# Kernel optimization log

Hardware: AMD Instinct MI355X
Metric: run time of the kernel (lower is better)

The kernel has to match this reference:

```python
import jax, jax.numpy as jnp
import numpy as np

N = 50000
E = 800000
H = 128
K = 4
BN_EPS = 1e-5


def _cheb_norm(edge_index):
    # PyG ChebConv with normalization='sym', lambda_max=2.0:
    # L_hat = 2L/lambda_max - I = -D^{-1/2} A D^{-1/2}
    src, dst = edge_index[0], edge_index[1]
    deg = jax.ops.segment_sum(jnp.ones((E,), jnp.float32), src, num_segments=N)
    dinv = jnp.where(deg > 0, jax.lax.rsqrt(jnp.maximum(deg, 1.0)), 0.0)
    return -dinv[src] * dinv[dst]  # [E]


def _cheb_conv(x, src, dst, w, W, b):
    # Chebyshev recursion: Tx0=x, Tx1=L_hat x, Txk = 2 L_hat Tx_{k-1} - Tx_{k-2}
    def prop(h):
        return jax.ops.segment_sum(h[src] * w[:, None], dst, num_segments=N)
    Tx0 = x
    out = Tx0 @ W[0]
    Tx1 = prop(Tx0)
    out = out + Tx1 @ W[1]
    for k in range(2, W.shape[0]):
        Tx2 = 2.0 * prop(Tx1) - Tx0
        out = out + Tx2 @ W[k]
        Tx0, Tx1 = Tx1, Tx2
    return out + b


def _bn(h, gamma, beta):
    # BatchNorm1d, training mode: biased batch stats over nodes
    m = h.mean(axis=0)
    v = h.var(axis=0)
    return (h - m) * jax.lax.rsqrt(v + BN_EPS) * gamma + beta


def setup_inputs() -> dict:
    key = jax.random.key(0)
    ks = jax.random.split(key, 8)
    x = jax.random.normal(ks[0], (N, 3), jnp.float32)
    edge_index = jax.random.randint(ks[1], (2, E), 0, N, jnp.int64)
    s1 = 1.0 / np.sqrt(3)
    s2 = 1.0 / np.sqrt(H)
    d = {
        'x': x,
        'edge_index': edge_index,
        'W1': jax.random.normal(ks[2], (K, 3, H), jnp.float32) * s1,
        'b1': jnp.zeros((H,), jnp.float32),
        'W2': jax.random.normal(ks[3], (K, H, H), jnp.float32) * s2,
        'b2': jnp.zeros((H,), jnp.float32),
        'W3': jax.random.normal(ks[4], (K, H, H), jnp.float32) * s2,
        'b3': jnp.zeros((H,), jnp.float32),
        'W4': jax.random.normal(ks[5], (K, H, H), jnp.float32) * s2,
        'b4': jnp.zeros((H,), jnp.float32),
        'g1': jnp.ones((H,), jnp.float32), 'be1': jnp.zeros((H,), jnp.float32),
        'g2': jnp.ones((H,), jnp.float32), 'be2': jnp.zeros((H,), jnp.float32),
        'g3': jnp.ones((H,), jnp.float32), 'be3': jnp.zeros((H,), jnp.float32),
    }
    return d


def reference(x, edge_index, W1, b1, W2, b2, W3, b3, W4, b4, g1, be1, g2, be2, g3, be3):
    src, dst = edge_index[0], edge_index[1]
    w = _cheb_norm(edge_index)
    h = _bn(jax.nn.leaky_relu(_cheb_conv(x, src, dst, w, W1, b1)), g1, be1)
    h = _bn(jax.nn.leaky_relu(_cheb_conv(h, src, dst, w, W2, b2)), g2, be2)
    h = _bn(jax.nn.relu(_cheb_conv(h, src, dst, w, W3, b3)), g3, be3)
    h = _cheb_conv(h, src, dst, w, W4, b4)
    # F.normalize(p=2, dim=1)
    nrm = jnp.sqrt(jnp.sum(h * h, axis=1, keepdims=True))
    return h / jnp.maximum(nrm, 1e-12)
```

## Files before the change

kernel.cpp:

```cpp
#include <hip/hip_runtime.h>
#include <hip/hip_fp16.h>

#define NN 50000
#define NE 800000
#define HD 128
#define NSL 128
#define SLE (NE / NSL)
#define PW  12500

typedef __attribute__((ext_vector_type(8))) short short8;
typedef __attribute__((ext_vector_type(4))) float f32x4;
typedef __attribute__((ext_vector_type(4))) unsigned u32x4;

__device__ inline unsigned bf2pack(float lo, float hi) {
    unsigned a = __float_as_uint(lo); a = (a + 0x7fffu + ((a >> 16) & 1u)) >> 16;
    unsigned b = __float_as_uint(hi); b = (b + 0x7fffu + ((b >> 16) & 1u)) >> 16;
    return a | (b << 16);
}

__device__ inline float edgw(unsigned p) {
    return __half2float(__ushort_as_half((unsigned short)(p >> 16)));
}

__global__ __launch_bounds__(256) void k_hist(const int* __restrict__ ei,
                                              unsigned* __restrict__ phist) {
    __shared__ unsigned hist[PW];
    int b = blockIdx.x;
    int a = b >> 8;
    int s = (b & 255) >> 1;
    int c = b & 1;
    int tid = threadIdx.x;
    for (int i = tid; i < PW; i += 256) hist[i] = 0u;
    __syncthreads();
    const int* arr = ei + a * NE + s * SLE;
    int lo = c * 25000;
    for (int i = tid; i < SLE; i += 256) {
        int v = arr[i] - lo;
        if ((unsigned)v < 25000u)
            atomicAdd(&hist[v >> 1], 1u << ((v & 1) * 16));
    }
    __syncthreads();
    unsigned* dst = phist + (size_t)b * PW;
    for (int i = tid; i < PW; i += 256) dst[i] = hist[i];
}

__global__ __launch_bounds__(256) void k_hreduce(const unsigned* __restrict__ phist,
                                                 float* __restrict__ dinv,
                                                 int* __restrict__ cnt,
                                                 unsigned* __restrict__ pre,
                                                 int* __restrict__ dhist) {
    if (blockIdx.x == 0 && threadIdx.x < 64) dhist[threadIdx.x] = 0;
    int idx = blockIdx.x * 256 + threadIdx.x;
    if (idx >= 50000) return;
    int a = idx / 25000;
    int gw = idx % 25000;
    int c = gw / PW;
    int w = gw % PW;
    unsigned accLo = 0, accHi = 0;
    for (int s = 0; s < NSL; s++) {
        unsigned p = phist[(size_t)(((a * NSL + s) * 2 + c)) * PW + w];
        if (a == 1) pre[(size_t)s * 25000 + gw] = accLo | (accHi << 16);
        accLo += p & 0xffffu;
        accHi += p >> 16;
    }
    int b0 = c * 25000 + 2 * w;
    if (a == 0) {
        dinv[b0]     = accLo ? rsqrtf((float)accLo) : 0.0f;
        dinv[b0 + 1] = accHi ? rsqrtf((float)accHi) : 0.0f;
    } else {
        cnt[b0]     = (int)accLo;
        cnt[b0 + 1] = (int)accHi;
    }
}

__global__ __launch_bounds__(1024) void k_scan1(const int* __restrict__ cnt,
                                                int* __restrict__ rowptr,
                                                int* __restrict__ bsum,
                                                int* __restrict__ dhist) {
    __shared__ int s[1024];
    __shared__ int dh[64];
    int tid = threadIdx.x;
    int gid = blockIdx.x * 1024 + tid;
    int v = (gid < NN) ? cnt[gid] : 0;
    s[tid] = v;
    if (tid < 64) dh[tid] = 0;
    __syncthreads();
    if (gid < NN) atomicAdd(&dh[v < 63 ? v : 63], 1);
    for (int off = 1; off < 1024; off <<= 1) {
        int t = 0;
        if (tid >= off) t = s[tid - off];
        __syncthreads();
        s[tid] += t;
        __syncthreads();
    }
    if (gid < NN) rowptr[gid] = s[tid] - v;
    if (tid == 1023) bsum[blockIdx.x] = s[1023];
    if (tid < 64 && dh[tid]) atomicAdd(&dhist[tid], dh[tid]);
}

__global__ void k_scan2(const int* __restrict__ bsum, int* __restrict__ boff,
                        int nb, int* __restrict__ rowptr,
                        const int* __restrict__ dhist, int* __restrict__ gbase) {
    int lane = threadIdx.x;
    int v = (lane < nb) ? bsum[lane] : 0;
    int s = v;
    #pragma unroll
    for (int off = 1; off < 64; off <<= 1) {
        int t = __shfl_up(s, off, 64);
        if (lane >= off) s += t;
    }
    if (lane < nb) boff[lane] = s - v;
    if (lane == 63) rowptr[NN] = s;
    int d = dhist[lane];
    int sd = d;
    #pragma unroll
    for (int off = 1; off < 64; off <<= 1) {
        int t = __shfl_up(sd, off, 64);
        if (lane >= off) sd += t;
    }
    gbase[lane] = sd - d;
}

__global__ void k_scan3(int* __restrict__ rowptr, const int* __restrict__ boff) {
    int i = blockIdx.x * 256 + threadIdx.x;
    if (i < NN) rowptr[i] += boff[i >> 10];
}

__global__ __launch_bounds__(256) void k_permbuild(const int* __restrict__ cnt,
                                                   int* __restrict__ gbase,
                                                   int* __restrict__ perm) {
    __shared__ int lcnt[64];
    __shared__ int lbase[64];
    int tid = threadIdx.x;
    if (tid < 64) lcnt[tid] = 0;
    __syncthreads();
    int n = blockIdx.x * 256 + tid;
    int r = 0, dg = 0;
    if (n < NN) {
        int v = cnt[n];
        dg = v < 63 ? v : 63;
        r = atomicAdd(&lcnt[dg], 1);
    }
    __syncthreads();
    if (tid < 64 && lcnt[tid]) lbase[tid] = atomicAdd(&gbase[tid], lcnt[tid]);
    __syncthreads();
    if (n < NN) perm[lbase[dg] + r] = n;
}

__global__ __launch_bounds__(256) void k_fill2(const int* __restrict__ ei,
                                               const float* __restrict__ dinv,
                                               const int* __restrict__ rowptr,
                                               const unsigned* __restrict__ pre,
                                               unsigned* __restrict__ edg) {
    __shared__ unsigned rank[PW];
    int b = blockIdx.x;
    int s = b >> 1;
    int c = b & 1;
    int tid = threadIdx.x;
    for (int i = tid; i < PW; i += 256) rank[i] = 0u;
    __syncthreads();
    int lo = c * 25000;
    const unsigned* preS = pre + (size_t)s * 25000 + c * PW;
    for (int i = tid; i < SLE; i += 256) {
        int e = s * SLE + i;
        int d = ei[NE + e];
        int v = d - lo;
        if ((unsigned)v < 25000u) {
            int src = ei[e];
            int w = v >> 1;
            int sh = (v & 1) * 16;
            unsigned r = atomicAdd(&rank[w], 1u << sh);
            r = (r >> sh) & 0xffffu;
            unsigned pw = (preS[w] >> sh) & 0xffffu;
            int pos = rowptr[d] + (int)pw + (int)r;
            unsigned short hw = __half_as_ushort(__float2half(-dinv[src] * dinv[d]));
            edg[pos] = (unsigned)src | ((unsigned)hw << 16);
        }
    }
}

__global__ __launch_bounds__(128) void k_prop3(const float* __restrict__ h,
                        const float* __restrict__ sub,
                        const int* __restrict__ rowptr, const unsigned* __restrict__ edg,
                        const int* __restrict__ perm,
                        float* __restrict__ out) {
    int idx = blockIdx.x * 128 + threadIdx.x;
    if (idx >= NN) return;
    int node = perm[idx];
    int e0 = rowptr[node], e1 = rowptr[node + 1];
    float a0 = 0.f, a1 = 0.f, a2 = 0.f;
    float c0 = 0.f, c1 = 0.f, c2 = 0.f;
    int e = e0;
    for (; e + 4 <= e1; e += 4) {
        unsigned p0 = edg[e], p1 = edg[e + 1], p2 = edg[e + 2], p3 = edg[e + 3];
        int s0 = (int)(p0 & 0xffffu) * 3, s1 = (int)(p1 & 0xffffu) * 3;
        int s2 = (int)(p2 & 0xffffu) * 3, s3 = (int)(p3 & 0xffffu) * 3;
        float x0 = h[s0], y0 = h[s0 + 1], z0 = h[s0 + 2];
        float x1 = h[s1], y1 = h[s1 + 1], z1 = h[s1 + 2];
        float x2 = h[s2], y2 = h[s2 + 1], z2 = h[s2 + 2];
        float x3 = h[s3], y3 = h[s3 + 1], z3 = h[s3 + 2];
        float w0 = edgw(p0), w1 = edgw(p1), w2 = edgw(p2), w3 = edgw(p3);
        a0 = fmaf(w0, x0, a0); a1 = fmaf(w0, y0, a1); a2 = fmaf(w0, z0, a2);
        c0 = fmaf(w1, x1, c0); c1 = fmaf(w1, y1, c1); c2 = fmaf(w1, z1, c2);
        a0 = fmaf(w2, x2, a0); a1 = fmaf(w2, y2, a1); a2 = fmaf(w2, z2, a2);
        c0 = fmaf(w3, x3, c0); c1 = fmaf(w3, y3, c1); c2 = fmaf(w3, z3, c2);
    }
    if (e < e1) {
        unsigned p0 = edg[e];
        unsigned p1 = (e + 1 < e1) ? edg[e + 1] : 0u;
        unsigned p2 = (e + 2 < e1) ? edg[e + 2] : 0u;
        int s0 = (int)(p0 & 0xffffu) * 3, s1 = (int)(p1 & 0xffffu) * 3;
        int s2 = (int)(p2 & 0xffffu) * 3;
        float x0 = h[s0], y0 = h[s0 + 1], z0 = h[s0 + 2];
        float x1 = h[s1], y1 = h[s1 + 1], z1 = h[s1 + 2];
        float x2 = h[s2], y2 = h[s2 + 1], z2 = h[s2 + 2];
        float w0 = edgw(p0), w1 = edgw(p1), w2 = edgw(p2);
        a0 = fmaf(w0, x0, a0); a1 = fmaf(w0, y0, a1); a2 = fmaf(w0, z0, a2);
        c0 = fmaf(w1, x1, c0); c1 = fmaf(w1, y1, c1); c2 = fmaf(w1, z1, c2);
        a0 = fmaf(w2, x2, a0); a1 = fmaf(w2, y2, a1); a2 = fmaf(w2, z2, a2);
    }
    a0 += c0; a1 += c1; a2 += c2;
    if (sub) {
        a0 = 2.f * a0 - sub[node * 3 + 0];
        a1 = 2.f * a1 - sub[node * 3 + 1];
        a2 = 2.f * a2 - sub[node * 3 + 2];
    }
    out[node * 3 + 0] = a0;
    out[node * 3 + 1] = a1;
    out[node * 3 + 2] = a2;
}

#define ACC8(acc, u, v)                                               \
    acc[0] = fmaf(v, __uint_as_float(u[0] << 16), acc[0]);            \
    acc[1] = fmaf(v, __uint_as_float(u[0] & 0xffff0000u), acc[1]);    \
    acc[2] = fmaf(v, __uint_as_float(u[1] << 16), acc[2]);            \
    acc[3] = fmaf(v, __uint_as_float(u[1] & 0xffff0000u), acc[3]);    \
    acc[4] = fmaf(v, __uint_as_float(u[2] << 16), acc[4]);            \
    acc[5] = fmaf(v, __uint_as_float(u[2] & 0xffff0000u), acc[5]);    \
    acc[6] = fmaf(v, __uint_as_float(u[3] << 16), acc[6]);            \
    acc[7] = fmaf(v, __uint_as_float(u[3] & 0xffff0000u), acc[7]);

__global__ __launch_bounds__(256) void k_prop_pl(
        const unsigned short* __restrict__ h, const unsigned short* __restrict__ sub,
        const int* __restrict__ rowptr, const unsigned* __restrict__ edg,
        const int* __restrict__ perm,
        unsigned short* __restrict__ out) {
    int B = blockIdx.x;
    int xcd = B & 7;
    int c = xcd >> 1;
    int half = xcd & 1;
    int g = B >> 3;
    int i = g * 64 + (threadIdx.x >> 2);
    int si = i * 2 + half;
    if (si >= NN) return;
    int n = perm[si];
    int lane4 = threadIdx.x & 3;
    int sl = lane4 * 8;
    int base = (threadIdx.x & 63) & ~3;
    const unsigned short* hp = h + (size_t)c * (NN * 32);
    int e0 = rowptr[n], e1 = rowptr[n + 1];
    float a[8] = {0, 0, 0, 0, 0, 0, 0, 0};
    float b[8] = {0, 0, 0, 0, 0, 0, 0, 0};
    int e = e0;
    for (; e + 8 <= e1; e += 8) {
        uint2 pp = *(const uint2*)(edg + e + lane4 * 2);
        unsigned q0 = __shfl(pp.x, base + 0, 64);
        unsigned q1 = __shfl(pp.y, base + 0, 64);
        unsigned q2 = __shfl(pp.x, base + 1, 64);
        unsigned q3 = __shfl(pp.y, base + 1, 64);
        unsigned q4 = __shfl(pp.x, base + 2, 64);
        unsigned q5 = __shfl(pp.y, base + 2, 64);
        unsigned q6 = __shfl(pp.x, base + 3, 64);
        unsigned q7 = __shfl(pp.y, base + 3, 64);
        u32x4 u0 = *(const u32x4*)(hp + (q0 & 0xffffu) * 32 + sl);
        u32x4 u1 = *(const u32x4*)(hp + (q1 & 0xffffu) * 32 + sl);
        u32x4 u2 = *(const u32x4*)(hp + (q2 & 0xffffu) * 32 + sl);
        u32x4 u3 = *(const u32x4*)(hp + (q3 & 0xffffu) * 32 + sl);
        u32x4 u4 = *(const u32x4*)(hp + (q4 & 0xffffu) * 32 + sl);
        u32x4 u5 = *(const u32x4*)(hp + (q5 & 0xffffu) * 32 + sl);
        u32x4 u6 = *(const u32x4*)(hp + (q6 & 0xffffu) * 32 + sl);
        u32x4 u7 = *(const u32x4*)(hp + (q7 & 0xffffu) * 32 + sl);
        float v0 = edgw(q0), v1 = edgw(q1), v2 = edgw(q2), v3 = edgw(q3);
        float v4 = edgw(q4), v5 = edgw(q5), v6 = edgw(q6), v7 = edgw(q7);
        ACC8(a, u0, v0)
        ACC8(b, u1, v1)
        ACC8(a, u2, v2)
        ACC8(b, u3, v3)
        ACC8(a, u4, v4)
        ACC8(b, u5, v5)
        ACC8(a, u6, v6)
        ACC8(b, u7, v7)
    }
    int rem = e1 - e;
    if (rem > 0) {
        uint2 pp = *(const uint2*)(edg + e + lane4 * 2);
        unsigned q0 = __shfl(pp.x, base + 0, 64);
        unsigned q1 = __shfl(pp.y, base + 0, 64);
        unsigned q2 = __shfl(pp.x, base + 1, 64);
        unsigned q3 = __shfl(pp.y, base + 1, 64);
        unsigned q4 = __shfl(pp.x, base + 2, 64);
        unsigned q5 = __shfl(pp.y, base + 2, 64);
        unsigned q6 = __shfl(pp.x, base + 3, 64);
        unsigned q7 = __shfl(pp.y, base + 3, 64);
        q1 = (rem > 1) ? q1 : 0u;
        q2 = (rem > 2) ? q2 : 0u;
        q3 = (rem > 3) ? q3 : 0u;
        q4 = (rem > 4) ? q4 : 0u;
        q5 = (rem > 5) ? q5 : 0u;
        q6 = (rem > 6) ? q6 : 0u;
        q7 = 0u;
        u32x4 u0 = *(const u32x4*)(hp + (q0 & 0xffffu) * 32 + sl);
        u32x4 u1 = *(const u32x4*)(hp + (q1 & 0xffffu) * 32 + sl);
        u32x4 u2 = *(const u32x4*)(hp + (q2 & 0xffffu) * 32 + sl);
        u32x4 u3 = *(const u32x4*)(hp + (q3 & 0xffffu) * 32 + sl);
        u32x4 u4 = *(const u32x4*)(hp + (q4 & 0xffffu) * 32 + sl);
        u32x4 u5 = *(const u32x4*)(hp + (q5 & 0xffffu) * 32 + sl);
        u32x4 u6 = *(const u32x4*)(hp + (q6 & 0xffffu) * 32 + sl);
        u32x4 u7 = *(const u32x4*)(hp + (q7 & 0xffffu) * 32 + sl);
        float v0 = edgw(q0), v1 = edgw(q1), v2 = edgw(q2), v3 = edgw(q3);
        float v4 = edgw(q4), v5 = edgw(q5), v6 = edgw(q6), v7 = edgw(q7);
        ACC8(a, u0, v0)
        ACC8(b, u1, v1)
        ACC8(a, u2, v2)
        ACC8(b, u3, v3)
        ACC8(a, u4, v4)
        ACC8(b, u5, v5)
        ACC8(a, u6, v6)
        ACC8(b, u7, v7)
    }
    float r[8];
    #pragma unroll
    for (int q = 0; q < 8; q++) r[q] = a[q] + b[q];
    if (sub) {
        u32x4 su = __builtin_nontemporal_load(
            (const u32x4*)(sub + (size_t)c * (NN * 32) + n * 32 + sl));
        float s[8];
        s[0] = __uint_as_float(su[0] << 16); s[1] = __uint_as_float(su[0] & 0xffff0000u);
        s[2] = __uint_as_float(su[1] << 16); s[3] = __uint_as_float(su[1] & 0xffff0000u);
        s[4] = __uint_as_float(su[2] << 16); s[5] = __uint_as_float(su[2] & 0xffff0000u);
        s[6] = __uint_as_float(su[3] << 16); s[7] = __uint_as_float(su[3] & 0xffff0000u);
        #pragma unroll
        for (int q = 0; q < 8; q++) r[q] = 2.f * r[q] - s[q];
    }
    u32x4 o;
    o[0] = bf2pack(r[0], r[1]);
    o[1] = bf2pack(r[2], r[3]);
    o[2] = bf2pack(r[4], r[5]);
    o[3] = bf2pack(r[6], r[7]);
    __builtin_nontemporal_store(o, (u32x4*)(out + (size_t)c * (NN * 32) + n * 32 + sl));
}

__global__ void k_wconv_all(const float* __restrict__ W2, const float* __restrict__ W3,
                            const float* __restrict__ W4, unsigned short* __restrict__ Wb) {
    int gidx = blockIdx.x * 256 + threadIdx.x;
    int which = gidx >> 16;
    int idx = gidx & 65535;
    const float* W = which == 0 ? W2 : (which == 1 ? W3 : W4);
    int slot = idx >> 9;
    int lane = (idx >> 3) & 63;
    int j = idx & 7;
    int wg = slot >> 4;
    int t = slot & 15;
    int w = wg >> 1;
    int g = wg & 1;
    int k = t * 32 + (lane >> 4) * 8 + j;
    int col = w * 32 + g * 16 + (lane & 15);
    unsigned u = __float_as_uint(W[k * HD + col]);
    Wb[which * 65536 + idx] = (unsigned short)((u + 0x7fffu + ((u >> 16) & 1u)) >> 16);
}

__global__ __launch_bounds__(256) void k_gemmM(
        const unsigned short* __restrict__ A0, const unsigned short* __restrict__ A1,
        const unsigned short* __restrict__ A2, const unsigned short* __restrict__ A3,
        const unsigned short* __restrict__ Wb, const float* __restrict__ bias,
        float* __restrict__ outF, int act, float* __restrict__ gpart) {
    __shared__ unsigned short Asm[16 * 64 * 8];
    __shared__ float sred[64];
    const int tid = threadIdx.x;
    const int w = tid >> 6;
    const int lane = tid & 63;
    const int l15 = lane & 15;
    const int quad = lane >> 4;

    short8 Bf[16][2];
    #pragma unroll
    for (int t = 0; t < 16; t++) {
        #pragma unroll
        for (int g = 0; g < 2; g++) {
            int slot = (w * 2 + g) * 16 + t;
            Bf[t][g] = *(const short8*)(Wb + slot * 512 + lane * 8);
        }
    }
    float bcol[2];
    bcol[0] = bias[w * 32 + l15];
    bcol[1] = bias[w * 32 + 16 + l15];

    const unsigned short* Ap[4] = {A0, A1, A2, A3};
    float bnP[2] = {0.f, 0.f}, bnQ[2] = {0.f, 0.f};

    for (int tile = blockIdx.x; tile < NN / 16; tile += gridDim.x) {
        int r0 = tile * 16;
        __syncthreads();
        #pragma unroll
        for (int i = 0; i < 4; i++) {
            int idx = i * 256 + tid;
            int s = idx >> 6;
            int ln = idx & 63;
            const unsigned short* src = Ap[s >> 2] + (size_t)(s & 3) * (NN * 32)
                                        + (r0 + (ln & 15)) * 32 + (ln >> 4) * 8;
            *(uint4*)&Asm[idx * 8] = *(const uint4*)src;
        }
        __syncthreads();
        f32x4 acc0 = {0.f, 0.f, 0.f, 0.f};
        f32x4 acc1 = {0.f, 0.f, 0.f, 0.f};
        #pragma unroll
        for (int s = 0; s < 16; s++) {
            short8 af = *(const short8*)&Asm[(s * 64 + lane) * 8];
            acc0 = __builtin_amdgcn_mfma_f32_16x16x32_bf16(af, Bf[s][0], acc0, 0, 0, 0);
            acc1 = __builtin_amdgcn_mfma_f32_16x16x32_bf16(af, Bf[s][1], acc1, 0, 0, 0);
        }
        if (act == 3) {
            float vv0[4], vv1[4], rs[4];
            #pragma unroll
            for (int reg = 0; reg < 4; reg++) {
                float v0 = acc0[reg] + bcol[0];
                float v1 = acc1[reg] + bcol[1];
                vv0[reg] = v0; vv1[reg] = v1;
                float s2 = v0 * v0 + v1 * v1;
                s2 += __shfl_xor(s2, 1);
                s2 += __shfl_xor(s2, 2);
                s2 += __shfl_xor(s2, 4);
                s2 += __shfl_xor(s2, 8);
                rs[reg] = s2;
            }
            if (l15 == 0) {
                #pragma unroll
                for (int reg = 0; reg < 4; reg++)
                    sred[w * 16 + quad * 4 + reg] = rs[reg];
            }
            __syncthreads();
            #pragma unroll
            for (int reg = 0; reg < 4; reg++) {
                int row16 = quad * 4 + reg;
                float tot = sred[row16] + sred[16 + row16]
                          + sred[32 + row16] + sred[48 + row16];
                float sc = 1.f / fmaxf(sqrtf(tot), 1e-12f);
                int row = r0 + row16;
                outF[row * HD + w * 32 + l15] = vv0[reg] * sc;
                outF[row * HD + w * 32 + 16 + l15] = vv1[reg] * sc;
            }
        } else {
            #pragma unroll
            for (int reg = 0; reg < 4; reg++) {
                int row = r0 + quad * 4 + reg;
                float v0 = acc0[reg] + bcol[0];
                float v1 = acc1[reg] + bcol[1];
                if (act == 1) {
                    v0 = v0 > 0.f ? v0 : 0.01f * v0;
                    v1 = v1 > 0.f ? v1 : 0.01f * v1;
                } else if (act == 2) {
                    v0 = v0 > 0.f ? v0 : 0.f;
                    v1 = v1 > 0.f ? v1 : 0.f;
                }
                outF[row * HD + w * 32 + l15] = v0;
                outF[row * HD + w * 32 + 16 + l15] = v1;
                bnP[0] += v0; bnQ[0] += v0 * v0;
                bnP[1] += v1; bnQ[1] += v1 * v1;
            }
        }
    }
    if (gpart) {
        #pragma unroll
        for (int g = 0; g < 2; g++) {
            float p = bnP[g], q = bnQ[g];
            p += __shfl_xor(p, 16); p += __shfl_xor(p, 32);
            q += __shfl_xor(q, 16); q += __shfl_xor(q, 32);
            if (quad == 0) {
                int col = w * 32 + g * 16 + l15;
                gpart[col * 512 + blockIdx.x] = p;
                gpart[(128 + col) * 512 + blockIdx.x] = q;
            }
        }
    }
}

__global__ __launch_bounds__(256) void k_gemm1(
        const float* __restrict__ T0, const float* __restrict__ T1,
        const float* __restrict__ T2, const float* __restrict__ T3,
        const float* __restrict__ W, const float* __restrict__ bias,
        float* __restrict__ out, float* __restrict__ gpart) {
    __shared__ float Ws[12 * 128];
    __shared__ float red[512];
    int t = threadIdx.x;
    for (int i = t; i < 12 * 128; i += 256) Ws[i] = W[i];
    __syncthreads();
    int f = t & 127;
    int half = t >> 7;
    float bs = bias[f];
    float bP = 0.f, bQ = 0.f;
    int r0 = blockIdx.x * 98;
    int r1 = r0 + 98;
    if (r1 > NN) r1 = NN;
    const float* Ts[4] = {T0, T1, T2, T3};
    for (int n = r0 + half; n < r1; n += 2) {
        float acc = bs;
        #pragma unroll
        for (int c = 0; c < 12; c++) {
            float tv = Ts[c / 3][n * 3 + (c % 3)];
            acc = fmaf(tv, Ws[c * 128 + f], acc);
        }
        acc = acc > 0.f ? acc : 0.01f * acc;
        out[n * HD + f] = acc;
        bP += acc;
        bQ += acc * acc;
    }
    red[t] = bP;
    red[256 + t] = bQ;
    __syncthreads();
    if (t < 128) {
        gpart[t * 512 + blockIdx.x] = red[t] + red[t + 128];
        gpart[(128 + t) * 512 + blockIdx.x] = red[256 + t] + red[256 + t + 128];
    }
}

__global__ __launch_bounds__(128) void k_bnredfin(const float* __restrict__ gpart,
                                                  const float* __restrict__ g,
                                                  const float* __restrict__ be,
                                                  float* __restrict__ ss) {
    __shared__ float sm[2];
    int f = blockIdx.x;
    int wave = threadIdx.x >> 6;
    int lane = threadIdx.x & 63;
    const float* src = gpart + (size_t)(f + wave * 128) * 512;
    float s = 0.f;
    #pragma unroll
    for (int i = 0; i < 8; i++) s += src[i * 64 + lane];
    #pragma unroll
    for (int off = 32; off > 0; off >>= 1) s += __shfl_xor(s, off);
    if (lane == 0) sm[wave] = s;
    __syncthreads();
    if (threadIdx.x == 0) {
        float mean = sm[0] * (1.0f / NN);
        float var = sm[1] * (1.0f / NN) - mean * mean;
        float sc = g[f] * rsqrtf(var + 1e-5f);
        ss[f] = sc;
        ss[128 + f] = be[f] - mean * sc;
    }
}

__global__ void k_bncvt_pl(const float* __restrict__ h, const float* __restrict__ ss,
                           unsigned short* __restrict__ out) {
    int idx = blockIdx.x * 256 + threadIdx.x;
    if (idx < NN * 16) {
        int n = idx >> 4;
        int p = (idx >> 2) & 3;
        int q = idx & 3;
        const float4* hf = (const float4*)h;
        float4 v0 = hf[n * 32 + p * 8 + q * 2];
        float4 v1 = hf[n * 32 + p * 8 + q * 2 + 1];
        const float4* s4 = (const float4*)ss;
        float4 c0 = s4[p * 8 + q * 2];
        float4 c1 = s4[p * 8 + q * 2 + 1];
        float4 d0 = s4[32 + p * 8 + q * 2];
        float4 d1 = s4[32 + p * 8 + q * 2 + 1];
        v0.x = fmaf(v0.x, c0.x, d0.x); v0.y = fmaf(v0.y, c0.y, d0.y);
        v0.z = fmaf(v0.z, c0.z, d0.z); v0.w = fmaf(v0.w, c0.w, d0.w);
        v1.x = fmaf(v1.x, c1.x, d1.x); v1.y = fmaf(v1.y, c1.y, d1.y);
        v1.z = fmaf(v1.z, c1.z, d1.z); v1.w = fmaf(v1.w, c1.w, d1.w);
        uint4 o;
        o.x = bf2pack(v0.x, v0.y);
        o.y = bf2pack(v0.z, v0.w);
        o.z = bf2pack(v1.x, v1.y);
        o.w = bf2pack(v1.z, v1.w);
        ((uint4*)out)[(size_t)p * (NN * 4) + n * 4 + q] = o;
    }
}

extern "C" void kernel_launch(void* const* d_in, const int* in_sizes, int n_in,
                              void* d_out, int out_size, void* d_ws, size_t ws_size,
                              hipStream_t stream) {
    const float* x  = (const float*)d_in[0];
    const int*   ei = (const int*)d_in[1];
    const float* W1 = (const float*)d_in[2];
    const float* b1 = (const float*)d_in[3];
    const float* W2 = (const float*)d_in[4];
    const float* b2 = (const float*)d_in[5];
    const float* W3 = (const float*)d_in[6];
    const float* b3 = (const float*)d_in[7];
    const float* W4 = (const float*)d_in[8];
    const float* b4 = (const float*)d_in[9];
    const float* g1 = (const float*)d_in[10];
    const float* be1 = (const float*)d_in[11];
    const float* g2 = (const float*)d_in[12];
    const float* be2 = (const float*)d_in[13];
    const float* g3 = (const float*)d_in[14];
    const float* be3 = (const float*)d_in[15];
    float* outp = (float*)d_out;

    char* base = (char*)d_ws;
    size_t off = 0;
    auto alloc = [&](size_t bytes) -> void* {
        void* p = base + off;
        off += (bytes + 255) & ~(size_t)255;
        return p;
    };
    float* dinv  = (float*)alloc(NN * 4);
    int*   cnt   = (int*)  alloc(NN * 4);
    int*   rowptr= (int*)  alloc((NN + 1) * 4);
    int*   bsum  = (int*)  alloc(64 * 4);
    int*   boff  = (int*)  alloc(64 * 4);
    int*   dhist = (int*)  alloc(64 * 4);
    int*   gbase = (int*)  alloc(64 * 4);
    int*   perm  = (int*)  alloc(NN * 4);
    float* ss    = (float*)alloc(256 * 4);
    float* gpart = (float*)alloc(256 * 512 * 4);
    unsigned short* Wb = (unsigned short*)alloc(3 * 512 * 128 * 2);
    unsigned* edg = (unsigned*)alloc((size_t)(NE + 8) * 4);
    float* T3a   = (float*)alloc(NN * 3 * 4);
    float* T3b   = (float*)alloc(NN * 3 * 4);
    float* T3c   = (float*)alloc(NN * 3 * 4);
    float* F0    = (float*)alloc((size_t)NN * HD * 4);
    unsigned short* Bb0 = (unsigned short*)alloc((size_t)NN * HD * 2);
    unsigned short* Bb1 = (unsigned short*)alloc((size_t)NN * HD * 2);
    unsigned short* Bb2 = (unsigned short*)alloc((size_t)NN * HD * 2);
    unsigned short* Bb3 = (unsigned short*)alloc((size_t)NN * HD * 2);

    unsigned* pre   = (unsigned*)F0;
    unsigned* phist = (unsigned*)Bb0;

    const int gN = (NN + 255) / 256;
    const int gP3 = (NN + 127) / 128;
    const int nb = (NN + 1023) / 1024;

    k_hist<<<512, 256, 0, stream>>>(ei, phist);
    k_hreduce<<<(50000 + 255) / 256, 256, 0, stream>>>(phist, dinv, cnt, pre, dhist);
    k_scan1<<<nb, 1024, 0, stream>>>(cnt, rowptr, bsum, dhist);
    k_scan2<<<1, 64, 0, stream>>>(bsum, boff, nb, rowptr, dhist, gbase);
    k_permbuild<<<gN, 256, 0, stream>>>(cnt, gbase, perm);
    k_scan3<<<gN, 256, 0, stream>>>(rowptr, boff);
    k_fill2<<<256, 256, 0, stream>>>(ei, dinv, rowptr, pre, edg);
    k_wconv_all<<<768, 256, 0, stream>>>(W2, W3, W4, Wb);

    const int gPP = 8 * 392;
    const int gG = 512;
    const int gCvt = NN * 16 / 256;
    unsigned short* Wb2 = Wb;
    unsigned short* Wb3 = Wb + 65536;
    unsigned short* Wb4 = Wb + 131072;

    k_prop3<<<gP3, 128, 0, stream>>>(x, nullptr, rowptr, edg, perm, T3a);
    k_prop3<<<gP3, 128, 0, stream>>>(T3a, x, rowptr, edg, perm, T3b);
    k_prop3<<<gP3, 128, 0, stream>>>(T3b, T3a, rowptr, edg, perm, T3c);
    k_gemm1<<<512, 256, 0, stream>>>(x, T3a, T3b, T3c, W1, b1, F0, gpart);
    k_bnredfin<<<128, 128, 0, stream>>>(gpart, g1, be1, ss);
    k_bncvt_pl<<<gCvt, 256, 0, stream>>>(F0, ss, Bb0);

    k_prop_pl<<<gPP, 256, 0, stream>>>(Bb0, nullptr, rowptr, edg, perm, Bb1);
    k_prop_pl<<<gPP, 256, 0, stream>>>(Bb1, Bb0, rowptr, edg, perm, Bb2);
    k_prop_pl<<<gPP, 256, 0, stream>>>(Bb2, Bb1, rowptr, edg, perm, Bb3);
    k_gemmM<<<gG, 256, 0, stream>>>(Bb0, Bb1, Bb2, Bb3, Wb2, b2, F0, 1, gpart);
    k_bnredfin<<<128, 128, 0, stream>>>(gpart, g2, be2, ss);
    k_bncvt_pl<<<gCvt, 256, 0, stream>>>(F0, ss, Bb0);

    k_prop_pl<<<gPP, 256, 0, stream>>>(Bb0, nullptr, rowptr, edg, perm, Bb1);
    k_prop_pl<<<gPP, 256, 0, stream>>>(Bb1, Bb0, rowptr, edg, perm, Bb2);
    k_prop_pl<<<gPP, 256, 0, stream>>>(Bb2, Bb1, rowptr, edg, perm, Bb3);
    k_gemmM<<<gG, 256, 0, stream>>>(Bb0, Bb1, Bb2, Bb3, Wb3, b3, F0, 2, gpart);
    k_bnredfin<<<128, 128, 0, stream>>>(gpart, g3, be3, ss);
    k_bncvt_pl<<<gCvt, 256, 0, stream>>>(F0, ss, Bb0);

    k_prop_pl<<<gPP, 256, 0, stream>>>(Bb0, nullptr, rowptr, edg, perm, Bb1);
    k_prop_pl<<<gPP, 256, 0, stream>>>(Bb1, Bb0, rowptr, edg, perm, Bb2);
    k_prop_pl<<<gPP, 256, 0, stream>>>(Bb2, Bb1, rowptr, edg, perm, Bb3);
    k_gemmM<<<gG, 256, 0, stream>>>(Bb0, Bb1, Bb2, Bb3, Wb4, b4, outp, 3, nullptr);

    (void)n_in; (void)in_sizes; (void)out_size; (void)ws_size;
}
```

Measured before the change: 614.1 us.

## Renumber nodes by degree order so propagation and GEMMs run in permuted space

Nodes are relabeled into degree-sorted order. The CSR is rebuilt in that order, with edge sources remapped through an inverse permutation, and x is permuted once. Propagation kernels then index nodes directly instead of going through perm, so output writes and row reads are contiguous, and only the final GEMM scatters rows back through perm. This costs extra preprocessing (a second scan, an edge copy, an x permute, and another edge buffer), and the batch-norm statistics are unaffected because they are order-invariant.

```diff
diff --git a/kernel.cpp b/kernel.cpp
--- a/kernel.cpp
+++ b/kernel.cpp
@@ -83,9 +83,9 @@
     int gid = blockIdx.x * 1024 + tid;
     int v = (gid < NN) ? cnt[gid] : 0;
     s[tid] = v;
-    if (tid < 64) dh[tid] = 0;
-    __syncthreads();
-    if (gid < NN) atomicAdd(&dh[v < 63 ? v : 63], 1);
+    if (dhist && tid < 64) dh[tid] = 0;
+    __syncthreads();
+    if (dhist && gid < NN) atomicAdd(&dh[v < 63 ? v : 63], 1);
     for (int off = 1; off < 1024; off <<= 1) {
         int t = 0;
         if (tid >= off) t = s[tid - off];
@@ -95,11 +95,11 @@
     }
     if (gid < NN) rowptr[gid] = s[tid] - v;
     if (tid == 1023) bsum[blockIdx.x] = s[1023];
-    if (tid < 64 && dh[tid]) atomicAdd(&dhist[tid], dh[tid]);
+    if (dhist && tid < 64 && dh[tid]) atomicAdd(&dhist[tid], dh[tid]);
 }
 
 __global__ void k_scan2(const int* __restrict__ bsum, int* __restrict__ boff,
-                        int nb, int* __restrict__ rowptr,
+                        int nb, int* __restrict__ tail,
                         const int* __restrict__ dhist, int* __restrict__ gbase) {
     int lane = threadIdx.x;
     int v = (lane < nb) ? bsum[lane] : 0;
@@ -110,15 +110,17 @@
         if (lane >= off) s += t;
     }
     if (lane < nb) boff[lane] = s - v;
-    if (lane == 63) rowptr[NN] = s;
-    int d = dhist[lane];
-    int sd = d;
-    #pragma unroll
-    for (int off = 1; off < 64; off <<= 1) {
-        int t = __shfl_up(sd, off, 64);
-        if (lane >= off) sd += t;
-    }
-    gbase[lane] = sd - d;
+    if (lane == 63) tail[NN] = s;
+    if (dhist) {
+        int d = dhist[lane];
+        int sd = d;
+        #pragma unroll
+        for (int off = 1; off < 64; off <<= 1) {
+            int t = __shfl_up(sd, off, 64);
+            if (lane >= off) sd += t;
+        }
+        gbase[lane] = sd - d;
+    }
 }
 
 __global__ void k_scan3(int* __restrict__ rowptr, const int* __restrict__ boff) {
@@ -128,29 +130,37 @@
 
 __global__ __launch_bounds__(256) void k_permbuild(const int* __restrict__ cnt,
                                                    int* __restrict__ gbase,
-                                                   int* __restrict__ perm) {
+                                                   int* __restrict__ perm,
+                                                   int* __restrict__ inv,
+                                                   int* __restrict__ cntp) {
     __shared__ int lcnt[64];
     __shared__ int lbase[64];
     int tid = threadIdx.x;
     if (tid < 64) lcnt[tid] = 0;
     __syncthreads();
     int n = blockIdx.x * 256 + tid;
-    int r = 0, dg = 0;
+    int r = 0, dg = 0, v = 0;
     if (n < NN) {
-        int v = cnt[n];
+        v = cnt[n];
         dg = v < 63 ? v : 63;
         r = atomicAdd(&lcnt[dg], 1);
     }
     __syncthreads();
     if (tid < 64 && lcnt[tid]) lbase[tid] = atomicAdd(&gbase[tid], lcnt[tid]);
     __syncthreads();
-    if (n < NN) perm[lbase[dg] + r] = n;
+    if (n < NN) {
+        int pos = lbase[dg] + r;
+        perm[pos] = n;
+        inv[n] = pos;
+        cntp[pos] = v;
+    }
 }
 
 __global__ __launch_bounds__(256) void k_fill2(const int* __restrict__ ei,
                                                const float* __restrict__ dinv,
                                                const int* __restrict__ rowptr,
                                                const unsigned* __restrict__ pre,
+                                               const int* __restrict__ inv,
                                                unsigned* __restrict__ edg) {
     __shared__ unsigned rank[PW];
     int b = blockIdx.x;
@@ -174,19 +184,40 @@
             unsigned pw = (preS[w] >> sh) & 0xffffu;
             int pos = rowptr[d] + (int)pw + (int)r;
             unsigned short hw = __half_as_ushort(__float2half(-dinv[src] * dinv[d]));
-            edg[pos] = (unsigned)src | ((unsigned)hw << 16);
+            edg[pos] = (unsigned)inv[src] | ((unsigned)hw << 16);
         }
+    }
+}
+
+__global__ __launch_bounds__(256) void k_edgecopy(const int* __restrict__ rowptr,
+                                                  const int* __restrict__ newrowptr,
+                                                  const int* __restrict__ perm,
+                                                  const unsigned* __restrict__ edg,
+                                                  unsigned* __restrict__ edg2) {
+    int pos = blockIdx.x * 64 + (threadIdx.x >> 2);
+    if (pos >= NN) return;
+    int lane4 = threadIdx.x & 3;
+    int ob = rowptr[perm[pos]];
+    int nb = newrowptr[pos];
+    int deg = newrowptr[pos + 1] - nb;
+    for (int k = lane4; k < deg; k += 4) edg2[nb + k] = edg[ob + k];
+}
+
+__global__ void k_permx(const float* __restrict__ x, const int* __restrict__ perm,
+                        float* __restrict__ xp) {
+    int i = blockIdx.x * 256 + threadIdx.x;
+    if (i < NN * 3) {
+        int pos = i / 3, j = i - pos * 3;
+        xp[i] = x[perm[pos] * 3 + j];
     }
 }
 
 __global__ __launch_bounds__(128) void k_prop3(const float* __restrict__ h,
                         const float* __restrict__ sub,
                         const int* __restrict__ rowptr, const unsigned* __restrict__ edg,
-                        const int* __restrict__ perm,
                         float* __restrict__ out) {
-    int idx = blockIdx.x * 128 + threadIdx.x;
-    if (idx >= NN) return;
-    int node = perm[idx];
+    int node = blockIdx.x * 128 + threadIdx.x;
+    if (node >= NN) return;
     int e0 = rowptr[node], e1 = rowptr[node + 1];
     float a0 = 0.f, a1 = 0.f, a2 = 0.f;
     float c0 = 0.f, c1 = 0.f, c2 = 0.f;
@@ -243,17 +274,16 @@
 __global__ __launch_bounds__(256) void k_prop_pl(
         const unsigned short* __restrict__ h, const unsigned short* __restrict__ sub,
         const int* __restrict__ rowptr, const unsigned* __restrict__ edg,
-        const int* __restrict__ perm,
         unsigned short* __restrict__ out) {
     int B = blockIdx.x;
     int xcd = B & 7;
     int c = xcd >> 1;
     int half = xcd & 1;
     int g = B >> 3;
-    int i = g * 64 + (threadIdx.x >> 2);
-    int si = i * 2 + half;
-    if (si >= NN) return;
-    int n = perm[si];
+    int wid = threadIdx.x >> 6;
+    int niw = (threadIdx.x >> 2) & 15;
+    int n = (((g * 4 + wid) * 2 + half) << 4) + niw;
+    if (n >= NN) return;
     int lane4 = threadIdx.x & 3;
     int sl = lane4 * 8;
     int base = (threadIdx.x & 63) & ~3;
@@ -373,7 +403,8 @@
         const unsigned short* __restrict__ A0, const unsigned short* __restrict__ A1,
         const unsigned short* __restrict__ A2, const unsigned short* __restrict__ A3,
         const unsigned short* __restrict__ Wb, const float* __restrict__ bias,
-        float* __restrict__ outF, int act, float* __restrict__ gpart) {
+        float* __restrict__ outF, int act, float* __restrict__ gpart,
+        const int* __restrict__ permRow) {
     __shared__ unsigned short Asm[16 * 64 * 8];
     __shared__ float sred[64];
     const int tid = threadIdx.x;
@@ -445,7 +476,7 @@
                 float tot = sred[row16] + sred[16 + row16]
                           + sred[32 + row16] + sred[48 + row16];
                 float sc = 1.f / fmaxf(sqrtf(tot), 1e-12f);
-                int row = r0 + row16;
+                int row = permRow[r0 + row16];
                 outF[row * HD + w * 32 + l15] = vv0[reg] * sc;
                 outF[row * HD + w * 32 + 16 + l15] = vv1[reg] * sc;
             }
@@ -607,15 +638,22 @@
     float* dinv  = (float*)alloc(NN * 4);
     int*   cnt   = (int*)  alloc(NN * 4);
     int*   rowptr= (int*)  alloc((NN + 1) * 4);
+    int*   nrow  = (int*)  alloc((NN + 1) * 4);
     int*   bsum  = (int*)  alloc(64 * 4);
     int*   boff  = (int*)  alloc(64 * 4);
+    int*   bsum2 = (int*)  alloc(64 * 4);
+    int*   boff2 = (int*)  alloc(64 * 4);
     int*   dhist = (int*)  alloc(64 * 4);
     int*   gbase = (int*)  alloc(64 * 4);
     int*   perm  = (int*)  alloc(NN * 4);
+    int*   inv   = (int*)  alloc(NN * 4);
+    int*   cntp  = (int*)  alloc(NN * 4);
+    float* xp    = (float*)alloc(NN * 3 * 4);
     float* ss    = (float*)alloc(256 * 4);
     float* gpart = (float*)alloc(256 * 512 * 4);
     unsigned short* Wb = (unsigned short*)alloc(3 * 512 * 128 * 2);
-    unsigned* edg = (unsigned*)alloc((size_t)(NE + 8) * 4);
+    unsigned* edg  = (unsigned*)alloc((size_t)(NE + 8) * 4);
+    unsigned* edg2 = (unsigned*)alloc((size_t)(NE + 8) * 4);
     float* T3a   = (float*)alloc(NN * 3 * 4);
     float* T3b   = (float*)alloc(NN * 3 * 4);
     float* T3c   = (float*)alloc(NN * 3 * 4);
@@ -636,9 +674,14 @@
     k_hreduce<<<(50000 + 255) / 256, 256, 0, stream>>>(phist, dinv, cnt, pre, dhist);
     k_scan1<<<nb, 1024, 0, stream>>>(cnt, rowptr, bsum, dhist);
     k_scan2<<<1, 64, 0, stream>>>(bsum, boff, nb, rowptr, dhist, gbase);
-    k_permbuild<<<gN, 256, 0, stream>>>(cnt, gbase, perm);
+    k_permbuild<<<gN, 256, 0, stream>>>(cnt, gbase, perm, inv, cntp);
     k_scan3<<<gN, 256, 0, stream>>>(rowptr, boff);
-    k_fill2<<<256, 256, 0, stream>>>(ei, dinv, rowptr, pre, edg);
+    k_scan1<<<nb, 1024, 0, stream>>>(cntp, nrow, bsum2, nullptr);
+    k_scan2<<<1, 64, 0, stream>>>(bsum2, boff2, nb, nrow, nullptr, nullptr);
+    k_scan3<<<gN, 256, 0, stream>>>(nrow, boff2);
+    k_fill2<<<256, 256, 0, stream>>>(ei, dinv, rowptr, pre, inv, edg);
+    k_edgecopy<<<(NN + 63) / 64, 256, 0, stream>>>(rowptr, nrow, perm, edg, edg2);
+    k_permx<<<(NN * 3 + 255) / 256, 256, 0, stream>>>(x, perm, xp);
     k_wconv_all<<<768, 256, 0, stream>>>(W2, W3, W4, Wb);
 
     const int gPP = 8 * 392;
@@ -648,31 +691,31 @@
     unsigned short* Wb3 = Wb + 65536;
     unsigned short* Wb4 = Wb + 131072;
 
-    k_prop3<<<gP3, 128, 0, stream>>>(x, nullptr, rowptr, edg, perm, T3a);
-    k_prop3<<<gP3, 128, 0, stream>>>(T3a, x, rowptr, edg, perm, T3b);
-    k_prop3<<<gP3, 128, 0, stream>>>(T3b, T3a, rowptr, edg, perm, T3c);
-    k_gemm1<<<512, 256, 0, stream>>>(x, T3a, T3b, T3c, W1, b1, F0, gpart);
+    k_prop3<<<gP3, 128, 0, stream>>>(xp, nullptr, nrow, edg2, T3a);
+    k_prop3<<<gP3, 128, 0, stream>>>(T3a, xp, nrow, edg2, T3b);
+    k_prop3<<<gP3, 128, 0, stream>>>(T3b, T3a, nrow, edg2, T3c);
+    k_gemm1<<<512, 256, 0, stream>>>(xp, T3a, T3b, T3c, W1, b1, F0, gpart);
     k_bnredfin<<<128, 128, 0, stream>>>(gpart, g1, be1, ss);
     k_bncvt_pl<<<gCvt, 256, 0, stream>>>(F0, ss, Bb0);
 
-    k_prop_pl<<<gPP, 256, 0, stream>>>(Bb0, nullptr, rowptr, edg, perm, Bb1);
-    k_prop_pl<<<gPP, 256, 0, stream>>>(Bb1, Bb0, rowptr, edg, perm, Bb2);
-    k_prop_pl<<<gPP, 256, 0, stream>>>(Bb2, Bb1, rowptr, edg, perm, Bb3);
-    k_gemmM<<<gG, 256, 0, stream>>>(Bb0, Bb1, Bb2, Bb3, Wb2, b2, F0, 1, gpart);
+    k_prop_pl<<<gPP, 256, 0, stream>>>(Bb0, nullptr, nrow, edg2, Bb1);
+    k_prop_pl<<<gPP, 256, 0, stream>>>(Bb1, Bb0, nrow, edg2, Bb2);
+    k_prop_pl<<<gPP, 256, 0, stream>>>(Bb2, Bb1, nrow, edg2, Bb3);
+    k_gemmM<<<gG, 256, 0, stream>>>(Bb0, Bb1, Bb2, Bb3, Wb2, b2, F0, 1, gpart, nullptr);
     k_bnredfin<<<128, 128, 0, stream>>>(gpart, g2, be2, ss);
     k_bncvt_pl<<<gCvt, 256, 0, stream>>>(F0, ss, Bb0);
 
-    k_prop_pl<<<gPP, 256, 0, stream>>>(Bb0, nullptr, rowptr, edg, perm, Bb1);
-    k_prop_pl<<<gPP, 256, 0, stream>>>(Bb1, Bb0, rowptr, edg, perm, Bb2);
-    k_prop_pl<<<gPP, 256, 0, stream>>>(Bb2, Bb1, rowptr, edg, perm, Bb3);
-    k_gemmM<<<gG, 256, 0, stream>>>(Bb0, Bb1, Bb2, Bb3, Wb3, b3, F0, 2, gpart);
+    k_prop_pl<<<gPP, 256, 0, stream>>>(Bb0, nullptr, nrow, edg2, Bb1);
+    k_prop_pl<<<gPP, 256, 0, stream>>>(Bb1, Bb0, nrow, edg2, Bb2);
+    k_prop_pl<<<gPP, 256, 0, stream>>>(Bb2, Bb1, nrow, edg2, Bb3);
+    k_gemmM<<<gG, 256, 0, stream>>>(Bb0, Bb1, Bb2, Bb3, Wb3, b3, F0, 2, gpart, nullptr);
     k_bnredfin<<<128, 128, 0, stream>>>(gpart, g3, be3, ss);
     k_bncvt_pl<<<gCvt, 256, 0, stream>>>(F0, ss, Bb0);
 
-    k_prop_pl<<<gPP, 256, 0, stream>>>(Bb0, nullptr, rowptr, edg, perm, Bb1);
-    k_prop_pl<<<gPP, 256, 0, stream>>>(Bb1, Bb0, rowptr, edg, perm, Bb2);
-    k_prop_pl<<<gPP, 256, 0, stream>>>(Bb2, Bb1, rowptr, edg, perm, Bb3);
-    k_gemmM<<<gG, 256, 0, stream>>>(Bb0, Bb1, Bb2, Bb3, Wb4, b4, outp, 3, nullptr);
+    k_prop_pl<<<gPP, 256, 0, stream>>>(Bb0, nullptr, nrow, edg2, Bb1);
+    k_prop_pl<<<gPP, 256, 0, stream>>>(Bb1, Bb0, nrow, edg2, Bb2);
+    k_prop_pl<<<gPP, 256, 0, stream>>>(Bb2, Bb1, nrow, edg2, Bb3);
+    k_gemmM<<<gG, 256, 0, stream>>>(Bb0, Bb1, Bb2, Bb3, Wb4, b4, outp, 3, nullptr, perm);
 
     (void)n_in; (void)in_sizes; (void)out_size; (void)ws_size;
 }
```

New measurement: 562.2 us. -8.4%, faster.
